# Kernel tuning notes

Hardware: AMD Instinct MI355X
Metric: run time of the kernel (lower is better)

Reference implementation:

```python
import jax, jax.numpy as jnp
import numpy as np

N_NODES, N_EDGES, IN_DIM, H, D = 50000, 800000, 256, 4, 32
NEG_SLOPE = 0.2  # DGL GATv2Conv default


def setup_inputs() -> dict:
    key = jax.random.key(0)
    k = jax.random.split(key, 7)
    s_in = 1.0 / np.sqrt(IN_DIM)
    return {
        "h": jax.random.normal(k[0], (N_NODES, IN_DIM), jnp.float32),
        "src": jax.random.randint(k[1], (N_EDGES,), 0, N_NODES, jnp.int32),
        "dst": jax.random.randint(k[2], (N_EDGES,), 0, N_NODES, jnp.int32),
        "W_src": jax.random.normal(k[3], (IN_DIM, H * D), jnp.float32) * s_in,
        "b_src": jnp.zeros((H * D,), jnp.float32),
        "W_dst": jax.random.normal(k[4], (IN_DIM, H * D), jnp.float32) * s_in,
        "b_dst": jnp.zeros((H * D,), jnp.float32),
        "attn_a": jax.random.normal(k[5], (H, D), jnp.float32) * 0.1,
    }


def reference(h, src, dst, W_src, b_src, W_dst, b_dst, attn_a):
    """GATv2Conv (hop=1, get_attention=True) + reshape, as in TweetEmbedder.forward."""
    N = h.shape[0]
    el = (h @ W_src + b_src).reshape(N, H, D)  # fc_src, per-head
    er = (h @ W_dst + b_dst).reshape(N, H, D)  # fc_dst, per-head
    # edge scores: e_ij = a^T leaky_relu(W_src h_i + W_dst h_j)
    e = jax.nn.leaky_relu(el[src] + er[dst], NEG_SLOPE)          # (E, H, D)
    scores = jnp.einsum('ehd,hd->eh', e, attn_a)                  # (E, H)
    # edge softmax over incoming edges of each dst node
    m = jax.ops.segment_max(scores, dst, num_segments=N)          # (N, H)
    ex = jnp.exp(scores - m[dst])
    denom = jax.ops.segment_sum(ex, dst, num_segments=N)          # (N, H)
    a = ex / denom[dst]                                           # (E, H)
    # weighted scatter-aggregate of source messages
    out = jax.ops.segment_sum(a[:, :, None] * el[src], dst, num_segments=N)  # (N, H, D)
    return out.reshape(N, H * D), a[:, :, None]
```

## Files before the change

### kernel.cpp

```cpp
#include <hip/hip_runtime.h>
#include <cstdint>
#include <cstddef>

#define NNODES 50000
#define NEDGES 800000
#define INDIM  256
#define HD     128
#define NH     4
#define NEG    0.2f

#define SCAN_B ((NNODES + 255) / 256)

#define HIST_BLKS  ((NEDGES + 2047) / 2048)
#define CONVW_BLKS 64
#define GEMM_BLKS  ((NNODES + 127) / 128)
#define SCAT_BLKS  ((NEDGES + 2047) / 2048)

typedef __attribute__((ext_vector_type(8))) short   short8;
typedef __attribute__((ext_vector_type(8))) ushort  ushort8;
typedef __attribute__((ext_vector_type(4))) float   floatx4;

__device__ __forceinline__ ushort f2bf(float f) {
    unsigned u = __float_as_uint(f);
    unsigned r = u + 0x7fffu + ((u >> 16) & 1u);
    return (ushort)(r >> 16);
}
__device__ __forceinline__ float bf2f(ushort u) {
    return __uint_as_float(((unsigned)u) << 16);
}

__device__ __forceinline__ int swz(int c) { return c ^ ((c >> 4) & 7); }

__global__ __launch_bounds__(256) void fusedA_kernel(
        const int* __restrict__ dst, int* __restrict__ cnt_work,
        const float* __restrict__ Wsrc, const float* __restrict__ Wdst,
        ushort* __restrict__ Wt) {
    __shared__ float t[32][33];
    const int bid = blockIdx.x;
    const int tid = threadIdx.x;

    if (bid < HIST_BLKS) {
        int base = bid * 2048 + tid;
        int dd[8];
#pragma unroll
        for (int k = 0; k < 8; ++k) {
            int e = base + k * 256;
            dd[k] = (e < NEDGES) ? dst[e] : -1;
        }
#pragma unroll
        for (int k = 0; k < 8; ++k) {
            if (dd[k] >= 0) atomicAdd(cnt_work + dd[k], 1);
        }
    } else {
        int wb = bid - HIST_BLKS;
        int kb = (wb & 7) * 32, nb = (wb >> 3) * 32;
        int tx = tid & 31, ty = tid >> 5;
        for (int i = ty; i < 32; i += 8) {
            int k = kb + i, n = nb + tx;
            float v = (n < HD) ? Wsrc[(size_t)k * HD + n] : Wdst[(size_t)k * HD + (n - HD)];
            t[i][tx] = v;
        }
        __syncthreads();
        for (int i = ty; i < 32; i += 8) {
            int n = nb + i, k = kb + tx;
            Wt[(size_t)n * INDIM + k] = f2bf(t[tx][i]);
        }
    }
}

__global__ __launch_bounds__(256) void scan_partial_kernel(
        const int* __restrict__ cnt, int* __restrict__ partials) {
    __shared__ int lds[256];
    int i = blockIdx.x * 256 + threadIdx.x;
    lds[threadIdx.x] = (i < NNODES) ? cnt[i] : 0;
    __syncthreads();
    for (int off = 128; off > 0; off >>= 1) {
        if (threadIdx.x < off) lds[threadIdx.x] += lds[threadIdx.x + off];
        __syncthreads();
    }
    if (threadIdx.x == 0) partials[blockIdx.x] = lds[0];
}

__global__ __launch_bounds__(256) void scan_offsets_kernel(
        int* __restrict__ partials, int* __restrict__ rowptr) {
    __shared__ int lds[256];
    int t = threadIdx.x;
    int v = (t < SCAN_B) ? partials[t] : 0;
    lds[t] = v;
    __syncthreads();
    for (int off = 1; off < 256; off <<= 1) {
        int u = (t >= off) ? lds[t - off] : 0;
        __syncthreads();
        lds[t] += u;
        __syncthreads();
    }
    if (t < SCAN_B) partials[t] = lds[t] - v;
    if (t == 255) rowptr[NNODES] = lds[255];
}

__global__ __launch_bounds__(256) void scan_final_kernel(
        int* __restrict__ cnt_work, const int* __restrict__ partials,
        int* __restrict__ rowptr) {
    __shared__ int lds[256];
    int i = blockIdx.x * 256 + threadIdx.x;
    int t = threadIdx.x;
    int v = (i < NNODES) ? cnt_work[i] : 0;
    lds[t] = v;
    __syncthreads();
    for (int off = 1; off < 256; off <<= 1) {
        int u = (t >= off) ? lds[t - off] : 0;
        __syncthreads();
        lds[t] += u;
        __syncthreads();
    }
    if (i < NNODES) {
        int start = partials[blockIdx.x] + lds[t] - v;
        rowptr[i] = start;
        cnt_work[i] = start;
    }
}

__global__ __launch_bounds__(256, 2) void fusedB_kernel(
        const float* __restrict__ h, const ushort* __restrict__ Wt,
        const float* __restrict__ bsrc, const float* __restrict__ bdst,
        ushort* __restrict__ el_bf, float* __restrict__ er,
        const int* __restrict__ src, const int* __restrict__ dst,
        int* __restrict__ cnt_work, int2* __restrict__ epair) {
    __shared__ ushort As[512 * 8];
    __shared__ ushort Bs[1024 * 8];

    const int bid = blockIdx.x;
    const int tid = threadIdx.x;

    if (bid >= GEMM_BLKS) {
        int base = (bid - GEMM_BLKS) * 2048 + tid;
        int ss[8], dd[8], pos[8];
#pragma unroll
        for (int k = 0; k < 8; ++k) {
            int e = base + k * 256;
            if (e < NEDGES) { ss[k] = src[e]; dd[k] = dst[e]; } else dd[k] = -1;
        }
#pragma unroll
        for (int k = 0; k < 8; ++k) {
            if (dd[k] >= 0) pos[k] = atomicAdd(cnt_work + dd[k], 1);
        }
#pragma unroll
        for (int k = 0; k < 8; ++k) {
            int e = base + k * 256;
            if (dd[k] >= 0) epair[pos[k]] = make_int2(e, ss[k]);
        }
        return;
    }

    const int wave = tid >> 6, lane = tid & 63;
    const int row0 = bid * 128;
    const int l15  = lane & 15, quad = lane >> 4;

    floatx4 acc[2][16];
#pragma unroll
    for (int i = 0; i < 2; ++i)
#pragma unroll
        for (int j = 0; j < 16; ++j) acc[i][j] = (floatx4){0.f, 0.f, 0.f, 0.f};

    for (int kk = 0; kk < INDIM; kk += 32) {
#pragma unroll
        for (int it = 0; it < 2; ++it) {
            int idx = tid + it * 256;
            int r = idx >> 2;
            int kq = idx & 3;
            int c = (r >> 4) * 64 + kq * 16 + (r & 15);
            int grow = row0 + r;
            ushort8 aw = (ushort8){0,0,0,0,0,0,0,0};
            if (grow < NNODES) {
                const float* p = h + (size_t)grow * INDIM + kk + kq * 8;
                float4 v0 = *(const float4*)p;
                float4 v1 = *(const float4*)(p + 4);
                aw[0] = f2bf(v0.x); aw[1] = f2bf(v0.y); aw[2] = f2bf(v0.z); aw[3] = f2bf(v0.w);
                aw[4] = f2bf(v1.x); aw[5] = f2bf(v1.y); aw[6] = f2bf(v1.z); aw[7] = f2bf(v1.w);
            }
            *(ushort8*)(As + swz(c) * 8) = aw;
        }
#pragma unroll
        for (int it = 0; it < 4; ++it) {
            int idx = tid + it * 256;
            int r = idx >> 2;
            int kq = idx & 3;
            int c = (r >> 4) * 64 + kq * 16 + (r & 15);
            ushort8 bw = *(const ushort8*)(Wt + (size_t)r * INDIM + kk + kq * 8);
            *(ushort8*)(Bs + swz(c) * 8) = bw;
        }
        __syncthreads();

        short8 af[2];
#pragma unroll
        for (int tm = 0; tm < 2; ++tm) {
            int c = (wave * 2 + tm) * 64 + quad * 16 + l15;
            af[tm] = *(const short8*)(As + swz(c) * 8);
        }
#pragma unroll
        for (int tn = 0; tn < 16; ++tn) {
            int c = tn * 64 + quad * 16 + l15;
            short8 bfr = *(const short8*)(Bs + swz(c) * 8);
            acc[0][tn] = __builtin_amdgcn_mfma_f32_16x16x32_bf16(af[0], bfr, acc[0][tn], 0, 0, 0);
            acc[1][tn] = __builtin_amdgcn_mfma_f32_16x16x32_bf16(af[1], bfr, acc[1][tn], 0, 0, 0);
        }
        __syncthreads();
    }

#pragma unroll
    for (int tn = 0; tn < 8; ++tn) {
        int col = tn * 16 + l15;
        float bias = bsrc[col];
#pragma unroll
        for (int tm = 0; tm < 2; ++tm)
#pragma unroll
            for (int reg = 0; reg < 4; ++reg) {
                int row = row0 + wave * 32 + tm * 16 + quad * 4 + reg;
                if (row < NNODES)
                    el_bf[(size_t)row * HD + col] = f2bf(acc[tm][tn][reg] + bias);
            }
    }
#pragma unroll
    for (int tn = 8; tn < 16; ++tn) {
        int col = tn * 16 + l15 - HD;
        float bias = bdst[col];
#pragma unroll
        for (int tm = 0; tm < 2; ++tm)
#pragma unroll
            for (int reg = 0; reg < 4; ++reg) {
                int row = row0 + wave * 32 + tm * 16 + quad * 4 + reg;
                if (row < NNODES)
                    er[(size_t)row * HD + col] = acc[tm][tn][reg] + bias;
            }
    }
}

#define DEGCAP 128

__global__ __launch_bounds__(256) void node_fused_kernel(
        const ushort* __restrict__ el_bf, const float* __restrict__ er,
        const int* __restrict__ rowptr, const int2* __restrict__ epair,
        const float* __restrict__ attn,
        float* __restrict__ out_feat, float* __restrict__ out_a) {
    __shared__ float sp[4][DEGCAP * NH];

    const int wv = threadIdx.x >> 6;
    const int n = blockIdx.x * 4 + wv;
    if (n >= NNODES) return;
    const int lane = threadIdx.x & 63;
    const int hh = lane >> 4;
    const int lo = rowptr[n], hi = rowptr[n + 1];
    const int deg = hi - lo;
    float* spw = sp[wv];
    const int l2 = lane * 2;

    const float2 rv = *(const float2*)(er + (size_t)n * HD + l2);
    const float a0 = attn[l2], a1 = attn[l2 + 1];

    float m = -3.4e38f, lsum = 0.0f, acc0 = 0.0f, acc1 = 0.0f;

    if (deg > 0 && deg <= DEGCAP) {
        int jj0 = (lane & 15);
        if (jj0 >= deg) jj0 = deg - 1;
        int si = epair[lo + jj0].y;

        for (int base = 0; base < deg; base += 16) {
            ushort2 u[16];
#pragma unroll
            for (int j = 0; j < 16; ++j) {
                if (base + j < deg) {
                    int s = __builtin_amdgcn_readlane(si, j);
                    u[j] = *(const ushort2*)(el_bf + (size_t)s * HD + l2);
                }
            }
            int si_nxt = si;
            if (base + 16 < deg) {
                int jj = base + 16 + (lane & 15);
                if (jj >= deg) jj = deg - 1;
                si_nxt = epair[lo + jj].y;
            }
#pragma unroll
            for (int j = 0; j < 16; ++j) {
                if (base + j < deg) {
                    float evx = bf2f(u[j].x), evy = bf2f(u[j].y);
                    float x0 = evx + rv.x; x0 = fmaxf(x0, NEG * x0);
                    float x1 = evy + rv.y; x1 = fmaxf(x1, NEG * x1);
                    float p = x0 * a0 + x1 * a1;
                    p += __shfl_xor(p, 1, 16);
                    p += __shfl_xor(p, 2, 16);
                    p += __shfl_xor(p, 4, 16);
                    p += __shfl_xor(p, 8, 16);
                    if ((lane & 15) == 0) spw[(base + j) * NH + hh] = p;
                    if (p > m) {
                        float sc = __expf(m - p);
                        lsum = fmaf(lsum, sc, 1.0f);
                        acc0 = fmaf(acc0, sc, evx);
                        acc1 = fmaf(acc1, sc, evy);
                        m = p;
                    } else {
                        float w = __expf(p - m);
                        lsum += w;
                        acc0 = fmaf(w, evx, acc0);
                        acc1 = fmaf(w, evy, acc1);
                    }
                }
            }
            si = si_nxt;
        }
    } else if (deg > DEGCAP) {
        ushort2 u = {0,0};
        { int s_ = epair[lo].y; u = *(const ushort2*)(el_bf + (size_t)s_ * HD + l2); }
        for (int i = lo; i < hi; ++i) {
            float evx = bf2f(u.x), evy = bf2f(u.y);
            if (i + 1 < hi) { int s_ = epair[i + 1].y;
                u = *(const ushort2*)(el_bf + (size_t)s_ * HD + l2); }
            float x0 = evx + rv.x; x0 = fmaxf(x0, NEG * x0);
            float x1 = evy + rv.y; x1 = fmaxf(x1, NEG * x1);
            float p = x0 * a0 + x1 * a1;
            p += __shfl_xor(p, 1, 16);
            p += __shfl_xor(p, 2, 16);
            p += __shfl_xor(p, 4, 16);
            p += __shfl_xor(p, 8, 16);
            float mn = fmaxf(m, p);
            float sc = __expf(m - mn);
            float w  = __expf(p - mn);
            lsum = lsum * sc + w;
            acc0 = acc0 * sc + w * evx;
            acc1 = acc1 * sc + w * evy;
            m = mn;
        }
    }

    float2 o;
    if (deg == 0) { o.x = 0.0f; o.y = 0.0f; }
    else { float inv = 1.0f / lsum; o.x = acc0 * inv; o.y = acc1 * inv; }
    *(float2*)(out_feat + (size_t)n * HD + l2) = o;

    if (deg == 0) return;

    float inv = 1.0f / lsum;
    if (deg <= DEGCAP) {
        float mh   = __shfl(m,   (lane & 3) << 4, 64);
        float invh = __shfl(inv, (lane & 3) << 4, 64);
        for (int q = (lane >> 2); q < deg; q += 16) {
            int e = epair[lo + q].x;
            float p = spw[q * NH + (lane & 3)];
            out_a[(size_t)e * NH + (lane & 3)] = __expf(p - mh) * invh;
        }
    } else {
        for (int i = lo; i < hi; ++i) {
            int s_ = epair[i].y;
            ushort2 u = *(const ushort2*)(el_bf + (size_t)s_ * HD + l2);
            float evx = bf2f(u.x), evy = bf2f(u.y);
            float x0 = evx + rv.x; x0 = fmaxf(x0, NEG * x0);
            float x1 = evy + rv.y; x1 = fmaxf(x1, NEG * x1);
            float p = x0 * a0 + x1 * a1;
            p += __shfl_xor(p, 1, 16);
            p += __shfl_xor(p, 2, 16);
            p += __shfl_xor(p, 4, 16);
            p += __shfl_xor(p, 8, 16);
            if ((lane & 15) == 0) {
                int e = epair[i].x;
                out_a[(size_t)e * NH + hh] = __expf(p - m) * inv;
            }
        }
    }
}

extern "C" void kernel_launch(void* const* d_in, const int* in_sizes, int n_in,
                              void* d_out, int out_size, void* d_ws, size_t ws_size,
                              hipStream_t stream) {
    const float* h    = (const float*)d_in[0];
    const int*   src  = (const int*)d_in[1];
    const int*   dst  = (const int*)d_in[2];
    const float* Wsrc = (const float*)d_in[3];
    const float* bsrc = (const float*)d_in[4];
    const float* Wdst = (const float*)d_in[5];
    const float* bdst = (const float*)d_in[6];
    const float* attn = (const float*)d_in[7];

    float* out_feat = (float*)d_out;
    float* out_a    = out_feat + (size_t)NNODES * HD;

    float*  er       = (float*)d_ws;
    ushort* Wt       = (ushort*)(er + (size_t)NNODES * HD);
    ushort* el_bf    = Wt + 2 * HD * INDIM;
    int*    cnt_work = (int*)(el_bf + (size_t)NNODES * HD);
    int2*   epair    = (int2*)(cnt_work + NNODES);
    int*    rowptr   = (int*)(epair + NEDGES);
    int*    partials = rowptr + NNODES + 1;

    hipMemsetAsync(cnt_work, 0, NNODES * sizeof(int), stream);

    fusedA_kernel<<<HIST_BLKS + CONVW_BLKS, 256, 0, stream>>>(
        dst, cnt_work, Wsrc, Wdst, Wt);

    scan_partial_kernel<<<SCAN_B, 256, 0, stream>>>(cnt_work, partials);
    scan_offsets_kernel<<<1, 256, 0, stream>>>(partials, rowptr);
    scan_final_kernel<<<SCAN_B, 256, 0, stream>>>(cnt_work, partials, rowptr);

    fusedB_kernel<<<GEMM_BLKS + SCAT_BLKS, 256, 0, stream>>>(
        h, Wt, bsrc, bdst, el_bf, er, src, dst, cnt_work, epair);

    node_fused_kernel<<<(NNODES + 3) / 4, 256, 0, stream>>>(
        el_bf, er, rowptr, epair, attn, out_feat, out_a);
}
```

Measured before the change: 268.6 us.

## Replace CSR histogram+scan with fixed-capacity per-node buckets and overflow list

```diff
diff --git a/kernel.cpp b/kernel.cpp
--- a/kernel.cpp
+++ b/kernel.cpp
@@ -9,9 +9,9 @@
 #define NH     4
 #define NEG    0.2f
 
-#define SCAN_B ((NNODES + 255) / 256)
-
-#define HIST_BLKS  ((NEDGES + 2047) / 2048)
+#define BCAP   48
+#define OVFCAP 32768
+
 #define CONVW_BLKS 64
 #define GEMM_BLKS  ((NNODES + 127) / 128)
 #define SCAT_BLKS  ((NEDGES + 2047) / 2048)
@@ -31,92 +31,23 @@
 
 __device__ __forceinline__ int swz(int c) { return c ^ ((c >> 4) & 7); }
 
-__global__ __launch_bounds__(256) void fusedA_kernel(
-        const int* __restrict__ dst, int* __restrict__ cnt_work,
+__global__ __launch_bounds__(256) void convw_kernel(
         const float* __restrict__ Wsrc, const float* __restrict__ Wdst,
         ushort* __restrict__ Wt) {
     __shared__ float t[32][33];
-    const int bid = blockIdx.x;
+    const int wb = blockIdx.x;
     const int tid = threadIdx.x;
-
-    if (bid < HIST_BLKS) {
-        int base = bid * 2048 + tid;
-        int dd[8];
-#pragma unroll
-        for (int k = 0; k < 8; ++k) {
-            int e = base + k * 256;
-            dd[k] = (e < NEDGES) ? dst[e] : -1;
-        }
-#pragma unroll
-        for (int k = 0; k < 8; ++k) {
-            if (dd[k] >= 0) atomicAdd(cnt_work + dd[k], 1);
-        }
-    } else {
-        int wb = bid - HIST_BLKS;
-        int kb = (wb & 7) * 32, nb = (wb >> 3) * 32;
-        int tx = tid & 31, ty = tid >> 5;
-        for (int i = ty; i < 32; i += 8) {
-            int k = kb + i, n = nb + tx;
-            float v = (n < HD) ? Wsrc[(size_t)k * HD + n] : Wdst[(size_t)k * HD + (n - HD)];
-            t[i][tx] = v;
-        }
-        __syncthreads();
-        for (int i = ty; i < 32; i += 8) {
-            int n = nb + i, k = kb + tx;
-            Wt[(size_t)n * INDIM + k] = f2bf(t[tx][i]);
-        }
-    }
-}
-
-__global__ __launch_bounds__(256) void scan_partial_kernel(
-        const int* __restrict__ cnt, int* __restrict__ partials) {
-    __shared__ int lds[256];
-    int i = blockIdx.x * 256 + threadIdx.x;
-    lds[threadIdx.x] = (i < NNODES) ? cnt[i] : 0;
+    int kb = (wb & 7) * 32, nb = (wb >> 3) * 32;
+    int tx = tid & 31, ty = tid >> 5;
+    for (int i = ty; i < 32; i += 8) {
+        int k = kb + i, n = nb + tx;
+        float v = (n < HD) ? Wsrc[(size_t)k * HD + n] : Wdst[(size_t)k * HD + (n - HD)];
+        t[i][tx] = v;
+    }
     __syncthreads();
-    for (int off = 128; off > 0; off >>= 1) {
-        if (threadIdx.x < off) lds[threadIdx.x] += lds[threadIdx.x + off];
-        __syncthreads();
-    }
-    if (threadIdx.x == 0) partials[blockIdx.x] = lds[0];
-}
-
-__global__ __launch_bounds__(256) void scan_offsets_kernel(
-        int* __restrict__ partials, int* __restrict__ rowptr) {
-    __shared__ int lds[256];
-    int t = threadIdx.x;
-    int v = (t < SCAN_B) ? partials[t] : 0;
-    lds[t] = v;
-    __syncthreads();
-    for (int off = 1; off < 256; off <<= 1) {
-        int u = (t >= off) ? lds[t - off] : 0;
-        __syncthreads();
-        lds[t] += u;
-        __syncthreads();
-    }
-    if (t < SCAN_B) partials[t] = lds[t] - v;
-    if (t == 255) rowptr[NNODES] = lds[255];
-}
-
-__global__ __launch_bounds__(256) void scan_final_kernel(
-        int* __restrict__ cnt_work, const int* __restrict__ partials,
-        int* __restrict__ rowptr) {
-    __shared__ int lds[256];
-    int i = blockIdx.x * 256 + threadIdx.x;
-    int t = threadIdx.x;
-    int v = (i < NNODES) ? cnt_work[i] : 0;
-    lds[t] = v;
-    __syncthreads();
-    for (int off = 1; off < 256; off <<= 1) {
-        int u = (t >= off) ? lds[t - off] : 0;
-        __syncthreads();
-        lds[t] += u;
-        __syncthreads();
-    }
-    if (i < NNODES) {
-        int start = partials[blockIdx.x] + lds[t] - v;
-        rowptr[i] = start;
-        cnt_work[i] = start;
+    for (int i = ty; i < 32; i += 8) {
+        int n = nb + i, k = kb + tx;
+        Wt[(size_t)n * INDIM + k] = f2bf(t[tx][i]);
     }
 }
 
@@ -125,7 +56,8 @@
         const float* __restrict__ bsrc, const float* __restrict__ bdst,
         ushort* __restrict__ el_bf, float* __restrict__ er,
         const int* __restrict__ src, const int* __restrict__ dst,
-        int* __restrict__ cnt_work, int2* __restrict__ epair) {
+        int* __restrict__ cnt_work, int2* __restrict__ bucket,
+        int* __restrict__ ovf_cnt, int4* __restrict__ ovf) {
     __shared__ ushort As[512 * 8];
     __shared__ ushort Bs[1024 * 8];
 
@@ -146,8 +78,15 @@
         }
 #pragma unroll
         for (int k = 0; k < 8; ++k) {
-            int e = base + k * 256;
-            if (dd[k] >= 0) epair[pos[k]] = make_int2(e, ss[k]);
+            if (dd[k] >= 0) {
+                int e = base + k * 256;
+                if (pos[k] < BCAP) {
+                    bucket[(size_t)dd[k] * BCAP + pos[k]] = make_int2(e, ss[k]);
+                } else {
+                    int o = atomicAdd(ovf_cnt, 1);
+                    if (o < OVFCAP) ovf[o] = make_int4(e, ss[k], dd[k], 0);
+                }
+            }
         }
         return;
     }
@@ -235,34 +174,33 @@
     }
 }
 
-#define DEGCAP 128
-
 __global__ __launch_bounds__(256) void node_fused_kernel(
-        const ushort* __restrict__ el_bf, const float* __restrict__ er,
-        const int* __restrict__ rowptr, const int2* __restrict__ epair,
-        const float* __restrict__ attn,
-        float* __restrict__ out_feat, float* __restrict__ out_a) {
-    __shared__ float sp[4][DEGCAP * NH];
+        const ushort* __restrict__ el_bf, float* __restrict__ erout,
+        const int* __restrict__ cnt, const int2* __restrict__ bucket,
+        const int* __restrict__ ovf_cnt, const int4* __restrict__ ovf,
+        const float* __restrict__ attn, float* __restrict__ out_a) {
+    __shared__ float sp[4][BCAP * NH];
 
     const int wv = threadIdx.x >> 6;
     const int n = blockIdx.x * 4 + wv;
     if (n >= NNODES) return;
     const int lane = threadIdx.x & 63;
     const int hh = lane >> 4;
-    const int lo = rowptr[n], hi = rowptr[n + 1];
-    const int deg = hi - lo;
+    const int degf = cnt[n];
+    const int deg = (degf < BCAP) ? degf : BCAP;
+    const int2* bkt = bucket + (size_t)n * BCAP;
     float* spw = sp[wv];
     const int l2 = lane * 2;
 
-    const float2 rv = *(const float2*)(er + (size_t)n * HD + l2);
+    const float2 rv = *(const float2*)(erout + (size_t)n * HD + l2);
     const float a0 = attn[l2], a1 = attn[l2 + 1];
 
     float m = -3.4e38f, lsum = 0.0f, acc0 = 0.0f, acc1 = 0.0f;
 
-    if (deg > 0 && deg <= DEGCAP) {
+    if (deg > 0) {
         int jj0 = (lane & 15);
         if (jj0 >= deg) jj0 = deg - 1;
-        int si = epair[lo + jj0].y;
+        int si = bkt[jj0].y;
 
         for (int base = 0; base < deg; base += 16) {
             ushort2 u[16];
@@ -277,7 +215,7 @@
             if (base + 16 < deg) {
                 int jj = base + 16 + (lane & 15);
                 if (jj >= deg) jj = deg - 1;
-                si_nxt = epair[lo + jj].y;
+                si_nxt = bkt[jj].y;
             }
 #pragma unroll
             for (int j = 0; j < 16; ++j) {
@@ -307,13 +245,15 @@
             }
             si = si_nxt;
         }
-    } else if (deg > DEGCAP) {
-        ushort2 u = {0,0};
-        { int s_ = epair[lo].y; u = *(const ushort2*)(el_bf + (size_t)s_ * HD + l2); }
-        for (int i = lo; i < hi; ++i) {
-            float evx = bf2f(u.x), evy = bf2f(u.y);
-            if (i + 1 < hi) { int s_ = epair[i + 1].y;
-                u = *(const ushort2*)(el_bf + (size_t)s_ * HD + l2); }
+    }
+
+    if (degf > BCAP) {
+        int nov = *ovf_cnt; if (nov > OVFCAP) nov = OVFCAP;
+        for (int i = 0; i < nov; ++i) {
+            int4 t = ovf[i];
+            if (t.z != n) continue;
+            ushort2 uu = *(const ushort2*)(el_bf + (size_t)t.y * HD + l2);
+            float evx = bf2f(uu.x), evy = bf2f(uu.y);
             float x0 = evx + rv.x; x0 = fmaxf(x0, NEG * x0);
             float x1 = evy + rv.y; x1 = fmaxf(x1, NEG * x1);
             float p = x0 * a0 + x1 * a1;
@@ -321,37 +261,43 @@
             p += __shfl_xor(p, 2, 16);
             p += __shfl_xor(p, 4, 16);
             p += __shfl_xor(p, 8, 16);
-            float mn = fmaxf(m, p);
-            float sc = __expf(m - mn);
-            float w  = __expf(p - mn);
-            lsum = lsum * sc + w;
-            acc0 = acc0 * sc + w * evx;
-            acc1 = acc1 * sc + w * evy;
-            m = mn;
+            if (p > m) {
+                float sc = __expf(m - p);
+                lsum = fmaf(lsum, sc, 1.0f);
+                acc0 = fmaf(acc0, sc, evx);
+                acc1 = fmaf(acc1, sc, evy);
+                m = p;
+            } else {
+                float w = __expf(p - m);
+                lsum += w;
+                acc0 = fmaf(w, evx, acc0);
+                acc1 = fmaf(w, evy, acc1);
+            }
         }
     }
 
     float2 o;
-    if (deg == 0) { o.x = 0.0f; o.y = 0.0f; }
+    if (degf == 0) { o.x = 0.0f; o.y = 0.0f; }
     else { float inv = 1.0f / lsum; o.x = acc0 * inv; o.y = acc1 * inv; }
-    *(float2*)(out_feat + (size_t)n * HD + l2) = o;
-
-    if (deg == 0) return;
+    *(float2*)(erout + (size_t)n * HD + l2) = o;
+
+    if (degf == 0) return;
 
     float inv = 1.0f / lsum;
-    if (deg <= DEGCAP) {
-        float mh   = __shfl(m,   (lane & 3) << 4, 64);
-        float invh = __shfl(inv, (lane & 3) << 4, 64);
-        for (int q = (lane >> 2); q < deg; q += 16) {
-            int e = epair[lo + q].x;
-            float p = spw[q * NH + (lane & 3)];
-            out_a[(size_t)e * NH + (lane & 3)] = __expf(p - mh) * invh;
-        }
-    } else {
-        for (int i = lo; i < hi; ++i) {
-            int s_ = epair[i].y;
-            ushort2 u = *(const ushort2*)(el_bf + (size_t)s_ * HD + l2);
-            float evx = bf2f(u.x), evy = bf2f(u.y);
+    float mh   = __shfl(m,   (lane & 3) << 4, 64);
+    float invh = __shfl(inv, (lane & 3) << 4, 64);
+    for (int q = (lane >> 2); q < deg; q += 16) {
+        int e = bkt[q].x;
+        float p = spw[q * NH + (lane & 3)];
+        out_a[(size_t)e * NH + (lane & 3)] = __expf(p - mh) * invh;
+    }
+    if (degf > BCAP) {
+        int nov = *ovf_cnt; if (nov > OVFCAP) nov = OVFCAP;
+        for (int i = 0; i < nov; ++i) {
+            int4 t = ovf[i];
+            if (t.z != n) continue;
+            ushort2 uu = *(const ushort2*)(el_bf + (size_t)t.y * HD + l2);
+            float evx = bf2f(uu.x), evy = bf2f(uu.y);
             float x0 = evx + rv.x; x0 = fmaxf(x0, NEG * x0);
             float x1 = evy + rv.y; x1 = fmaxf(x1, NEG * x1);
             float p = x0 * a0 + x1 * a1;
@@ -359,10 +305,8 @@
             p += __shfl_xor(p, 2, 16);
             p += __shfl_xor(p, 4, 16);
             p += __shfl_xor(p, 8, 16);
-            if ((lane & 15) == 0) {
-                int e = epair[i].x;
-                out_a[(size_t)e * NH + hh] = __expf(p - m) * inv;
-            }
+            if ((lane & 15) == 0)
+                out_a[(size_t)t.x * NH + hh] = __expf(p - m) * inv;
         }
     }
 }
@@ -382,26 +326,20 @@
     float* out_feat = (float*)d_out;
     float* out_a    = out_feat + (size_t)NNODES * HD;
 
-    float*  er       = (float*)d_ws;
-    ushort* Wt       = (ushort*)(er + (size_t)NNODES * HD);
+    ushort* Wt       = (ushort*)d_ws;
     ushort* el_bf    = Wt + 2 * HD * INDIM;
     int*    cnt_work = (int*)(el_bf + (size_t)NNODES * HD);
-    int2*   epair    = (int2*)(cnt_work + NNODES);
-    int*    rowptr   = (int*)(epair + NEDGES);
-    int*    partials = rowptr + NNODES + 1;
-
-    hipMemsetAsync(cnt_work, 0, NNODES * sizeof(int), stream);
-
-    fusedA_kernel<<<HIST_BLKS + CONVW_BLKS, 256, 0, stream>>>(
-        dst, cnt_work, Wsrc, Wdst, Wt);
-
-    scan_partial_kernel<<<SCAN_B, 256, 0, stream>>>(cnt_work, partials);
-    scan_offsets_kernel<<<1, 256, 0, stream>>>(partials, rowptr);
-    scan_final_kernel<<<SCAN_B, 256, 0, stream>>>(cnt_work, partials, rowptr);
+    int*    ovf_cnt  = cnt_work + NNODES;
+    int4*   ovf      = (int4*)(ovf_cnt + 4);
+    int2*   bucket   = (int2*)(ovf + OVFCAP);
+
+    hipMemsetAsync(cnt_work, 0, (NNODES + 4) * sizeof(int), stream);
+
+    convw_kernel<<<CONVW_BLKS, 256, 0, stream>>>(Wsrc, Wdst, Wt);
 
     fusedB_kernel<<<GEMM_BLKS + SCAT_BLKS, 256, 0, stream>>>(
-        h, Wt, bsrc, bdst, el_bf, er, src, dst, cnt_work, epair);
+        h, Wt, bsrc, bdst, el_bf, out_feat, src, dst, cnt_work, bucket, ovf_cnt, ovf);
 
     node_fused_kernel<<<(NNODES + 3) / 4, 256, 0, stream>>>(
-        el_bf, er, rowptr, epair, attn, out_feat, out_a);
-}
+        el_bf, out_feat, cnt_work, bucket, ovf_cnt, ovf, attn, out_a);
+}
```

After: 271.5 us. Within noise of the previous version (+1.1%).

## Replace three-kernel scan with single-pass decoupled lookback scan, branchless exp2 softmax

Applied to the files above, without the earlier changes.

```diff
diff --git a/kernel.cpp b/kernel.cpp
--- a/kernel.cpp
+++ b/kernel.cpp
@@ -8,11 +8,13 @@
 #define HD     128
 #define NH     4
 #define NEG    0.2f
+#define LOG2E  1.44269504088896340736f
 
 #define SCAN_B ((NNODES + 255) / 256)
 
+#define CLR_BLKS   49
+#define CONVW_BLKS 64
 #define HIST_BLKS  ((NEDGES + 2047) / 2048)
-#define CONVW_BLKS 64
 #define GEMM_BLKS  ((NNODES + 127) / 128)
 #define SCAT_BLKS  ((NEDGES + 2047) / 2048)
 
@@ -31,79 +33,66 @@
 
 __device__ __forceinline__ int swz(int c) { return c ^ ((c >> 4) & 7); }
 
-__global__ __launch_bounds__(256) void fusedA_kernel(
-        const int* __restrict__ dst, int* __restrict__ cnt_work,
+__global__ __launch_bounds__(256) void fusedPre_kernel(
+        int* __restrict__ cnt_work, int* __restrict__ flags,
         const float* __restrict__ Wsrc, const float* __restrict__ Wdst,
         ushort* __restrict__ Wt) {
     __shared__ float t[32][33];
     const int bid = blockIdx.x;
     const int tid = threadIdx.x;
 
-    if (bid < HIST_BLKS) {
-        int base = bid * 2048 + tid;
-        int dd[8];
-#pragma unroll
-        for (int k = 0; k < 8; ++k) {
-            int e = base + k * 256;
-            dd[k] = (e < NEDGES) ? dst[e] : -1;
-        }
-#pragma unroll
-        for (int k = 0; k < 8; ++k) {
-            if (dd[k] >= 0) atomicAdd(cnt_work + dd[k], 1);
-        }
-    } else {
-        int wb = bid - HIST_BLKS;
-        int kb = (wb & 7) * 32, nb = (wb >> 3) * 32;
-        int tx = tid & 31, ty = tid >> 5;
-        for (int i = ty; i < 32; i += 8) {
-            int k = kb + i, n = nb + tx;
-            float v = (n < HD) ? Wsrc[(size_t)k * HD + n] : Wdst[(size_t)k * HD + (n - HD)];
-            t[i][tx] = v;
-        }
-        __syncthreads();
-        for (int i = ty; i < 32; i += 8) {
-            int n = nb + i, k = kb + tx;
-            Wt[(size_t)n * INDIM + k] = f2bf(t[tx][i]);
-        }
-    }
-}
-
-__global__ __launch_bounds__(256) void scan_partial_kernel(
-        const int* __restrict__ cnt, int* __restrict__ partials) {
+    if (bid < CLR_BLKS) {
+        int i = bid * 256 + tid;
+        if (i < (NNODES + 3) / 4)
+            ((int4*)cnt_work)[i] = make_int4(0, 0, 0, 0);
+        return;
+    }
+    if (bid == CLR_BLKS + CONVW_BLKS) {
+        if (tid < SCAN_B + 1) flags[tid] = 0;
+        return;
+    }
+    int wb = bid - CLR_BLKS;
+    int kb = (wb & 7) * 32, nb = (wb >> 3) * 32;
+    int tx = tid & 31, ty = tid >> 5;
+    for (int i = ty; i < 32; i += 8) {
+        int k = kb + i, n = nb + tx;
+        float v = (n < HD) ? Wsrc[(size_t)k * HD + n] : Wdst[(size_t)k * HD + (n - HD)];
+        t[i][tx] = v;
+    }
+    __syncthreads();
+    for (int i = ty; i < 32; i += 8) {
+        int n = nb + i, k = kb + tx;
+        Wt[(size_t)n * INDIM + k] = f2bf(t[tx][i]);
+    }
+}
+
+__global__ __launch_bounds__(256) void hist_kernel(
+        const int* __restrict__ dst, int* __restrict__ cnt_work) {
+    int base = blockIdx.x * 2048 + threadIdx.x;
+    int dd[8];
+#pragma unroll
+    for (int k = 0; k < 8; ++k) {
+        int e = base + k * 256;
+        dd[k] = (e < NEDGES) ? dst[e] : -1;
+    }
+#pragma unroll
+    for (int k = 0; k < 8; ++k) {
+        if (dd[k] >= 0) atomicAdd(cnt_work + dd[k], 1);
+    }
+}
+
+__global__ __launch_bounds__(256) void scan_lb_kernel(
+        int* __restrict__ cnt_work, int* __restrict__ rowptr,
+        int* __restrict__ flags, int* __restrict__ ticket) {
     __shared__ int lds[256];
-    int i = blockIdx.x * 256 + threadIdx.x;
-    lds[threadIdx.x] = (i < NNODES) ? cnt[i] : 0;
+    __shared__ int sh_tile, sh_prefix;
+    const int t = threadIdx.x;
+
+    if (t == 0) sh_tile = atomicAdd(ticket, 1);
     __syncthreads();
-    for (int off = 128; off > 0; off >>= 1) {
-        if (threadIdx.x < off) lds[threadIdx.x] += lds[threadIdx.x + off];
-        __syncthreads();
-    }
-    if (threadIdx.x == 0) partials[blockIdx.x] = lds[0];
-}
-
-__global__ __launch_bounds__(256) void scan_offsets_kernel(
-        int* __restrict__ partials, int* __restrict__ rowptr) {
-    __shared__ int lds[256];
-    int t = threadIdx.x;
-    int v = (t < SCAN_B) ? partials[t] : 0;
-    lds[t] = v;
-    __syncthreads();
-    for (int off = 1; off < 256; off <<= 1) {
-        int u = (t >= off) ? lds[t - off] : 0;
-        __syncthreads();
-        lds[t] += u;
-        __syncthreads();
-    }
-    if (t < SCAN_B) partials[t] = lds[t] - v;
-    if (t == 255) rowptr[NNODES] = lds[255];
-}
-
-__global__ __launch_bounds__(256) void scan_final_kernel(
-        int* __restrict__ cnt_work, const int* __restrict__ partials,
-        int* __restrict__ rowptr) {
-    __shared__ int lds[256];
-    int i = blockIdx.x * 256 + threadIdx.x;
-    int t = threadIdx.x;
+    const int tile = sh_tile;
+    const int i = tile * 256 + t;
+
     int v = (i < NNODES) ? cnt_work[i] : 0;
     lds[t] = v;
     __syncthreads();
@@ -113,11 +102,32 @@
         lds[t] += u;
         __syncthreads();
     }
+    const int excl = lds[t] - v;
+    const int bsum = lds[255];
+
+    if (t == 0) {
+        int prefix = 0;
+        if (tile > 0) {
+            int f;
+            while ((f = __hip_atomic_load(&flags[tile - 1], __ATOMIC_ACQUIRE,
+                                          __HIP_MEMORY_SCOPE_AGENT)) == 0) {
+                __builtin_amdgcn_s_sleep(1);
+            }
+            prefix = f - 1;
+        }
+        sh_prefix = prefix;
+        __hip_atomic_store(&flags[tile], prefix + bsum + 1, __ATOMIC_RELEASE,
+                           __HIP_MEMORY_SCOPE_AGENT);
+    }
+    __syncthreads();
+    const int prefix = sh_prefix;
+
     if (i < NNODES) {
-        int start = partials[blockIdx.x] + lds[t] - v;
+        int start = prefix + excl;
         rowptr[i] = start;
         cnt_work[i] = start;
     }
+    if (tile == SCAN_B - 1 && t == 255) rowptr[NNODES] = prefix + bsum;
 }
 
 __global__ __launch_bounds__(256, 2) void fusedB_kernel(
@@ -255,7 +265,7 @@
     const int l2 = lane * 2;
 
     const float2 rv = *(const float2*)(er + (size_t)n * HD + l2);
-    const float a0 = attn[l2], a1 = attn[l2 + 1];
+    const float a0 = attn[l2] * LOG2E, a1 = attn[l2 + 1] * LOG2E;
 
     float m = -3.4e38f, lsum = 0.0f, acc0 = 0.0f, acc1 = 0.0f;
 
@@ -291,18 +301,13 @@
                     p += __shfl_xor(p, 4, 16);
                     p += __shfl_xor(p, 8, 16);
                     if ((lane & 15) == 0) spw[(base + j) * NH + hh] = p;
-                    if (p > m) {
-                        float sc = __expf(m - p);
-                        lsum = fmaf(lsum, sc, 1.0f);
-                        acc0 = fmaf(acc0, sc, evx);
-                        acc1 = fmaf(acc1, sc, evy);
-                        m = p;
-                    } else {
-                        float w = __expf(p - m);
-                        lsum += w;
-                        acc0 = fmaf(w, evx, acc0);
-                        acc1 = fmaf(w, evy, acc1);
-                    }
+                    float mn = fmaxf(m, p);
+                    float sc = exp2f(m - mn);
+                    float w  = exp2f(p - mn);
+                    lsum = lsum * sc + w;
+                    acc0 = acc0 * sc + w * evx;
+                    acc1 = acc1 * sc + w * evy;
+                    m = mn;
                 }
             }
             si = si_nxt;
@@ -322,8 +327,8 @@
             p += __shfl_xor(p, 4, 16);
             p += __shfl_xor(p, 8, 16);
             float mn = fmaxf(m, p);
-            float sc = __expf(m - mn);
-            float w  = __expf(p - mn);
+            float sc = exp2f(m - mn);
+            float w  = exp2f(p - mn);
             lsum = lsum * sc + w;
             acc0 = acc0 * sc + w * evx;
             acc1 = acc1 * sc + w * evy;
@@ -345,7 +350,7 @@
         for (int q = (lane >> 2); q < deg; q += 16) {
             int e = epair[lo + q].x;
             float p = spw[q * NH + (lane & 3)];
-            out_a[(size_t)e * NH + (lane & 3)] = __expf(p - mh) * invh;
+            out_a[(size_t)e * NH + (lane & 3)] = exp2f(p - mh) * invh;
         }
     } else {
         for (int i = lo; i < hi; ++i) {
@@ -361,7 +366,7 @@
             p += __shfl_xor(p, 8, 16);
             if ((lane & 15) == 0) {
                 int e = epair[i].x;
-                out_a[(size_t)e * NH + hh] = __expf(p - m) * inv;
+                out_a[(size_t)e * NH + hh] = exp2f(p - m) * inv;
             }
         }
     }
@@ -388,16 +393,15 @@
     int*    cnt_work = (int*)(el_bf + (size_t)NNODES * HD);
     int2*   epair    = (int2*)(cnt_work + NNODES);
     int*    rowptr   = (int*)(epair + NEDGES);
-    int*    partials = rowptr + NNODES + 1;
-
-    hipMemsetAsync(cnt_work, 0, NNODES * sizeof(int), stream);
-
-    fusedA_kernel<<<HIST_BLKS + CONVW_BLKS, 256, 0, stream>>>(
-        dst, cnt_work, Wsrc, Wdst, Wt);
-
-    scan_partial_kernel<<<SCAN_B, 256, 0, stream>>>(cnt_work, partials);
-    scan_offsets_kernel<<<1, 256, 0, stream>>>(partials, rowptr);
-    scan_final_kernel<<<SCAN_B, 256, 0, stream>>>(cnt_work, partials, rowptr);
+    int*    flags    = rowptr + NNODES + 1;
+    int*    ticket   = flags + SCAN_B;
+
+    fusedPre_kernel<<<CLR_BLKS + CONVW_BLKS + 1, 256, 0, stream>>>(
+        cnt_work, flags, Wsrc, Wdst, Wt);
+
+    hist_kernel<<<HIST_BLKS, 256, 0, stream>>>(dst, cnt_work);
+
+    scan_lb_kernel<<<SCAN_B, 256, 0, stream>>>(cnt_work, rowptr, flags, ticket);
 
     fusedB_kernel<<<GEMM_BLKS + SCAT_BLKS, 256, 0, stream>>>(
         h, Wt, bsrc, bdst, el_bf, er, src, dst, cnt_work, epair);
```

Measured after the change: 628.4 us. 2.34x slower.
